# Optimization experiments

Hardware: AMD Instinct MI355X
Metric: run time of the kernel (lower is better)

Reference implementation:

```python
import jax, jax.numpy as jnp
import numpy as np

B, S, D = 2, 2048, 2048
H, KVH, HD = 16, 4, 128
NREP = H // KVH  # GQA repeat factor


def _rope(x, cos, sin):
    # x: [B,S,h,HD]; pairs (x[2k], x[2k+1]) form complex numbers
    xr = x[..., 0::2]
    xi = x[..., 1::2]
    cos = cos[None, :, None, :]  # [1,S,1,HD/2]
    sin = sin[None, :, None, :]
    out_r = xr * cos - xi * sin
    out_i = xr * sin + xi * cos
    return jnp.stack([out_r, out_i], axis=-1).reshape(x.shape)


def setup_inputs() -> dict:
    key = jax.random.key(0)
    ks = jax.random.split(key, 5)
    x = jax.random.normal(ks[0], (B, S, D), dtype=jnp.float32)
    # standard rotary frequencies
    inv_freq = 1.0 / (10000.0 ** (np.arange(0, HD, 2, dtype=np.float64) / HD))
    ang = np.outer(np.arange(S, dtype=np.float64), inv_freq)
    freqs_cos = jnp.asarray(np.cos(ang), dtype=jnp.float32)  # [S, HD/2]
    freqs_sin = jnp.asarray(np.sin(ang), dtype=jnp.float32)
    wq = jax.random.normal(ks[1], (D, H * HD), dtype=jnp.float32) * 0.02
    wk = jax.random.normal(ks[2], (D, KVH * HD), dtype=jnp.float32) * 0.02
    wv = jax.random.normal(ks[3], (D, KVH * HD), dtype=jnp.float32) * 0.02
    wo = jax.random.normal(ks[4], (H * HD, D), dtype=jnp.float32) * 0.02
    cache_k = jnp.zeros((B, S, KVH, HD), dtype=jnp.float32)
    cache_v = jnp.zeros((B, S, KVH, HD), dtype=jnp.float32)
    return {"x": x, "freqs_cos": freqs_cos, "freqs_sin": freqs_sin,
            "wq": wq, "wk": wk, "wv": wv, "wo": wo,
            "cache_k": cache_k, "cache_v": cache_v, "start_pos": 0}


def reference(x, freqs_cos, freqs_sin, wq, wk, wv, wo, cache_k, cache_v, start_pos):
    b, s, _ = x.shape
    xq = (x @ wq).reshape(b, s, H, HD)
    xk = (x @ wk).reshape(b, s, KVH, HD)
    xv = (x @ wv).reshape(b, s, KVH, HD)
    xq = _rope(xq, freqs_cos, freqs_sin)
    xk = _rope(xk, freqs_cos, freqs_sin)
    # KV cache update + slice (start_pos is a static Python int)
    ck = cache_k.at[:, start_pos:start_pos + s].set(xk)
    cv = cache_v.at[:, start_pos:start_pos + s].set(xv)
    keys = ck[:, :start_pos + s]    # [B,T,KVH,HD]
    vals = cv[:, :start_pos + s]
    # GQA without materializing repeat_kv: group query heads per kv head
    q = xq.reshape(b, s, KVH, NREP, HD)
    scores = jnp.einsum('bsknd,btkd->bknst', q, keys) / np.float32(np.sqrt(HD))
    probs = jax.nn.softmax(scores.astype(jnp.float32), axis=-1).astype(x.dtype)
    out = jnp.einsum('bknst,btkd->bsknd', probs, vals).reshape(b, s, H * HD)
    return out @ wo
```

## Files before the change

kernel.cpp:

```cpp
#include <hip/hip_runtime.h>
#include <stdint.h>
#include <stddef.h>

#define S_LEN  2048
#define NH     16
#define NKVH   4
#define HD_    128
#define DMODEL 2048
#define NQKV   3072
#define MROWS  4096

typedef __attribute__((ext_vector_type(8)))  __bf16 bf16x8;
typedef __attribute__((ext_vector_type(4)))  __bf16 bf16x4;
typedef __attribute__((ext_vector_type(4)))  float  f32x4;
typedef __attribute__((ext_vector_type(16))) float  f32x16;

#define MFMA16(a, b, c) __builtin_amdgcn_mfma_f32_16x16x32_bf16((a), (b), (c), 0, 0, 0)
#define MFMA32(a, b, c) __builtin_amdgcn_mfma_f32_32x32x16_bf16((a), (b), (c), 0, 0, 0)

__device__ __forceinline__ void gload16(const void* g, void* l) {
  __builtin_amdgcn_global_load_lds((const __attribute__((address_space(1))) void*)g,
                                   (__attribute__((address_space(3))) void*)l,
                                   16, 0, 0);
}

__device__ __forceinline__ float bf2f(uint16_t u) {
  uint32_t x = ((uint32_t)u) << 16;
  return __builtin_bit_cast(float, x);
}
__device__ __forceinline__ uint16_t f2bf(float f) {
  uint32_t u = __builtin_bit_cast(uint32_t, f);
  uint32_t r = (u + 0x7FFFu + ((u >> 16) & 1u)) >> 16;
  return (uint16_t)r;
}

__device__ __forceinline__ uint32_t cvtpk(float lo, float hi) {
  uint32_t d;
  asm("v_cvt_pk_bf16_f32 %0, %1, %2" : "=v"(d) : "v"(lo), "v"(hi));
  return d;
}
__device__ __forceinline__ void pswap(uint32_t& a, uint32_t& b) {
  asm("s_nop 1\n\tv_permlane32_swap_b32 %0, %1" : "+v"(a), "+v"(b));
}

__global__ void cvt_x_kernel(const float* __restrict__ x, __bf16* __restrict__ xb) {
  size_t i = (size_t)blockIdx.x * 256 + threadIdx.x;
  const float4* xv = (const float4*)x;
  float4 v = xv[i];
  bf16x4 o;
  o[0] = (__bf16)v.x; o[1] = (__bf16)v.y; o[2] = (__bf16)v.z; o[3] = (__bf16)v.w;
  *(bf16x4*)(xb + i * 4) = o;
}

__global__ void tw_kernel(const float* __restrict__ W, int ldw,
                          __bf16* __restrict__ WT, int ldt) {
  __shared__ float tile[64][65];
  const int k0 = blockIdx.x * 64, n0 = blockIdx.y * 64;
  const int tid = threadIdx.x;
#pragma unroll
  for (int r = 0; r < 16; ++r) {
    int idx = r * 256 + tid;
    int kr = idx >> 6, nc = idx & 63;
    tile[kr][nc] = W[(size_t)(k0 + kr) * ldw + n0 + nc];
  }
  __syncthreads();
#pragma unroll
  for (int r = 0; r < 16; ++r) {
    int idx = r * 256 + tid;
    int nr = idx >> 6, kc = idx & 63;
    WT[(size_t)(n0 + nr) * ldt + k0 + kc] = (__bf16)tile[kc][nr];
  }
}

template <int OUT_F32>
__global__ __launch_bounds__(256, 2) void gemm_kernel(
    const __bf16* __restrict__ A, int lda,
    const __bf16* __restrict__ Bt, int ldb,
    void* __restrict__ Cout, int ldc, int Kdim) {
  __shared__ __attribute__((aligned(16))) __bf16 As[128 * 64];
  __shared__ __attribute__((aligned(16))) __bf16 Bs[128 * 64];
  const int tid = threadIdx.x;
  const int w = tid >> 6, l = tid & 63, lg = l >> 4, lr = l & 15;
  const int wm = w >> 1, wn = w & 1;
  const int m0 = blockIdx.y * 128, n0 = blockIdx.x * 128;

  f32x4 acc[4][4] = {};

  for (int k0 = 0; k0 < Kdim; k0 += 64) {
#pragma unroll
    for (int t = 0; t < 4; ++t) {
      int o = (t * 256 + tid) * 16;
      int row = o >> 7;
      int slot = (o >> 4) & 7;
      int sw = slot ^ (row & 7);
      char* lbase = (char*)nullptr;
      lbase = (char*)As + t * 4096 + (w << 10);
      gload16(A + (size_t)(m0 + row) * lda + k0 + sw * 8, lbase);
      lbase = (char*)Bs + t * 4096 + (w << 10);
      gload16(Bt + (size_t)(n0 + row) * ldb + k0 + sw * 8, lbase);
    }
    __syncthreads();
#pragma unroll
    for (int c = 0; c < 2; ++c) {
      bf16x8 af[4];
#pragma unroll
      for (int mi = 0; mi < 4; ++mi) {
        int row = wm * 64 + mi * 16 + lr;
        int slot = (c * 4 + lg) ^ (row & 7);
        af[mi] = *(const bf16x8*)((const char*)As + row * 128 + slot * 16);
      }
#pragma unroll
      for (int ni = 0; ni < 4; ++ni) {
        int rn = wn * 64 + ni * 16 + lr;
        int slot = (c * 4 + lg) ^ (rn & 7);
        bf16x8 bfr = *(const bf16x8*)((const char*)Bs + rn * 128 + slot * 16);
#pragma unroll
        for (int mi = 0; mi < 4; ++mi)
          acc[mi][ni] = MFMA16(af[mi], bfr, acc[mi][ni]);
      }
    }
    __syncthreads();
  }

#pragma unroll
  for (int mi = 0; mi < 4; ++mi)
#pragma unroll
    for (int ni = 0; ni < 4; ++ni)
#pragma unroll
      for (int i = 0; i < 4; ++i) {
        int r = m0 + wm * 64 + mi * 16 + lg * 4 + i;
        int cc = n0 + wn * 64 + ni * 16 + lr;
        if (OUT_F32)
          ((float*)Cout)[(size_t)r * ldc + cc] = acc[mi][ni][i];
        else
          ((__bf16*)Cout)[(size_t)r * ldc + cc] = (__bf16)acc[mi][ni][i];
      }
}

__global__ void rope_kernel(__bf16* __restrict__ qkv,
                            const float* __restrict__ fc,
                            const float* __restrict__ fs) {
  const int row = blockIdx.x;
  const int s = row & (S_LEN - 1);
  const int tid = threadIdx.x;
  const float qscale = 0.08838834764831845f;
#pragma unroll
  for (int rep = 0; rep < 5; ++rep) {
    int pid = rep * 256 + tid;
    int col, j;
    float scale;
    if (pid < 1024) { int hh = pid >> 6; j = pid & 63; col = hh * HD_ + 2 * j; scale = qscale; }
    else { int p2 = pid - 1024; int kv = p2 >> 6; j = p2 & 63; col = DMODEL + kv * HD_ + 2 * j; scale = 1.0f; }
    uint32_t u = *(const uint32_t*)(qkv + (size_t)row * NQKV + col);
    float xr = bf2f((uint16_t)(u & 0xFFFFu));
    float xi = bf2f((uint16_t)(u >> 16));
    float c = fc[s * 64 + j], sn = fs[s * 64 + j];
    float orr = (xr * c - xi * sn) * scale;
    float oi  = (xr * sn + xi * c) * scale;
    uint32_t res = (uint32_t)f2bf(orr) | ((uint32_t)f2bf(oi) << 16);
    *(uint32_t*)(qkv + (size_t)row * NQKV + col) = res;
  }
}

__global__ void vt_kernel(const __bf16* __restrict__ qkv, __bf16* __restrict__ VT) {
  __shared__ uint16_t tile[64][66];
  const int bkv = blockIdx.z;
  const int b = bkv >> 2, kv = bkv & 3;
  const int s0 = blockIdx.x * 64, d0 = blockIdx.y * 64;
  const int tid = threadIdx.x;
#pragma unroll
  for (int r = 0; r < 16; ++r) {
    int idx = r * 256 + tid;
    int sr = idx >> 6, dc = idx & 63;
    tile[sr][dc] = *(const uint16_t*)(qkv + (size_t)(b * S_LEN + s0 + sr) * NQKV +
                                      (DMODEL + NKVH * HD_) + kv * HD_ + d0 + dc);
  }
  __syncthreads();
#pragma unroll
  for (int r = 0; r < 16; ++r) {
    int idx = r * 256 + tid;
    int dr = idx >> 6, sc = idx & 63;
    *(uint16_t*)(VT + (size_t)(bkv * HD_ + d0 + dr) * S_LEN + s0 + sc) = tile[sc][dr];
  }
}

__global__ __launch_bounds__(256, 2) void attn_kernel(
    const __bf16* __restrict__ qkv, const __bf16* __restrict__ VT,
    __bf16* __restrict__ out) {
  __shared__ __attribute__((aligned(16))) __bf16 Ks[64 * 128];
  __shared__ __attribute__((aligned(16))) __bf16 Vs[128 * 64];
  const int tid = threadIdx.x;
  const int w = tid >> 6, l = tid & 63;
  const int qc = l & 31, hi = l >> 5;
  const int bh = blockIdx.y;
  const int b = bh >> 4, h = bh & 15, kvh = h >> 2;
  const int q0 = blockIdx.x * 128 + w * 32;

  bf16x8 aq[8];
#pragma unroll
  for (int c = 0; c < 8; ++c)
    aq[c] = *(const bf16x8*)(qkv + (size_t)(b * S_LEN + q0 + qc) * NQKV +
                             h * HD_ + c * 16 + hi * 8);

  f32x16 o_acc[4] = {};
  float m = -1e30f, lsum = 0.0f;

  const __bf16* Kbase = qkv + (size_t)b * S_LEN * NQKV + DMODEL + kvh * HD_;
  const __bf16* Vbase = VT + (size_t)(b * NKVH + kvh) * (HD_ * S_LEN);

  typedef union { uint32_t u[4]; bf16x8 v; } pfrag_t;

  for (int kt = 0; kt < S_LEN / 64; ++kt) {
#pragma unroll
    for (int t = 0; t < 4; ++t) {
      int o = (t * 256 + tid) * 16;
      {
        int row = o >> 8; int slot = (o >> 4) & 15; int sw = slot ^ (row & 7);
        gload16(Kbase + (size_t)(kt * 64 + row) * NQKV + sw * 8,
                (char*)Ks + t * 4096 + (w << 10));
      }
      {
        int row = o >> 7; int slot = (o >> 4) & 7; int sw = slot ^ (row & 7);
        gload16(Vbase + (size_t)row * S_LEN + kt * 64 + sw * 8,
                (char*)Vs + t * 4096 + (w << 10));
      }
    }
    __syncthreads();

    f32x16 st[2] = {};
    __builtin_amdgcn_s_setprio(1);
#pragma unroll
    for (int t = 0; t < 2; ++t) {
#pragma unroll
      for (int c = 0; c < 8; ++c) {
        int row = t * 32 + qc;
        int slot = (c * 2 + hi) ^ (row & 7);
        bf16x8 kf = *(const bf16x8*)((const char*)Ks + row * 256 + slot * 16);
        st[t] = MFMA32(kf, aq[c], st[t]);
      }
    }
    __builtin_amdgcn_s_setprio(0);

    float pm = st[0][0];
#pragma unroll
    for (int t = 0; t < 2; ++t)
#pragma unroll
      for (int r = 0; r < 16; ++r) pm = fmaxf(pm, st[t][r]);
    pm = fmaxf(pm, __shfl_xor(pm, 32));

    if (__any(pm - m > 8.0f)) {
      float mn = fmaxf(m, pm);
      float sf = __expf(m - mn);
      lsum *= sf;
#pragma unroll
      for (int dt = 0; dt < 4; ++dt)
#pragma unroll
        for (int r = 0; r < 16; ++r) o_acc[dt][r] *= sf;
      m = mn;
    }

    float rsum = 0.0f;
#pragma unroll
    for (int t = 0; t < 2; ++t)
#pragma unroll
      for (int r = 0; r < 16; ++r) {
        st[t][r] = __expf(st[t][r] - m);
        rsum += st[t][r];
      }
    rsum += __shfl_xor(rsum, 32);
    lsum += rsum;

    pfrag_t pf[4];
#pragma unroll
    for (int t = 0; t < 2; ++t)
#pragma unroll
      for (int half = 0; half < 2; ++half) {
        int bs = half * 8;
        uint32_t x0 = cvtpk(st[t][bs + 0], st[t][bs + 1]);
        uint32_t y0 = cvtpk(st[t][bs + 4], st[t][bs + 5]);
        uint32_t x1 = cvtpk(st[t][bs + 2], st[t][bs + 3]);
        uint32_t y1 = cvtpk(st[t][bs + 6], st[t][bs + 7]);
        pswap(x0, y0);
        pswap(x1, y1);
        pf[t * 2 + half].u[0] = x0;
        pf[t * 2 + half].u[1] = x1;
        pf[t * 2 + half].u[2] = y0;
        pf[t * 2 + half].u[3] = y1;
      }

    __builtin_amdgcn_s_setprio(1);
#pragma unroll
    for (int dt = 0; dt < 4; ++dt) {
#pragma unroll
      for (int ks = 0; ks < 4; ++ks) {
        int row = dt * 32 + qc;
        int slot = (ks * 2 + hi) ^ (row & 7);
        bf16x8 vf = *(const bf16x8*)((const char*)Vs + row * 128 + slot * 16);
        o_acc[dt] = MFMA32(vf, pf[ks].v, o_acc[dt]);
      }
    }
    __builtin_amdgcn_s_setprio(0);
    __syncthreads();
  }

  float rinv = 1.0f / lsum;
  const size_t orow = (size_t)(b * S_LEN + q0 + qc) * DMODEL + h * HD_;
#pragma unroll
  for (int dt = 0; dt < 4; ++dt)
#pragma unroll
    for (int rg = 0; rg < 4; ++rg) {
      bf16x4 ov;
#pragma unroll
      for (int i = 0; i < 4; ++i)
        ov[i] = (__bf16)(o_acc[dt][rg * 4 + i] * rinv);
      int d = dt * 32 + rg * 8 + hi * 4;
      *(bf16x4*)(out + orow + d) = ov;
    }
}

extern "C" void kernel_launch(void* const* d_in, const int* in_sizes, int n_in,
                              void* d_out, int out_size, void* d_ws, size_t ws_size,
                              hipStream_t stream) {
  const float* x  = (const float*)d_in[0];
  const float* fc = (const float*)d_in[1];
  const float* fs = (const float*)d_in[2];
  const float* wq = (const float*)d_in[3];
  const float* wk = (const float*)d_in[4];
  const float* wv = (const float*)d_in[5];
  const float* wo = (const float*)d_in[6];

  char* ws = (char*)d_ws;
  __bf16* xb    = (__bf16*)(ws);
  __bf16* wqkvT = (__bf16*)(ws + (16u << 20));
  __bf16* woT   = (__bf16*)(ws + (28u << 20));
  __bf16* qkv   = (__bf16*)(ws + (36u << 20));
  __bf16* VT    = (__bf16*)(ws + (60u << 20));

  cvt_x_kernel<<<8192, 256, 0, stream>>>(x, xb);
  {
    dim3 g(32, 32); tw_kernel<<<g, 256, 0, stream>>>(wq, 2048, wqkvT, 2048);
  }
  {
    dim3 g(32, 8);
    tw_kernel<<<g, 256, 0, stream>>>(wk, 512, wqkvT + (size_t)2048 * 2048, 2048);
    tw_kernel<<<g, 256, 0, stream>>>(wv, 512, wqkvT + (size_t)2560 * 2048, 2048);
  }
  {
    dim3 g(32, 32); tw_kernel<<<g, 256, 0, stream>>>(wo, 2048, woT, 2048);
  }
  {
    dim3 g(NQKV / 128, MROWS / 128);
    gemm_kernel<0><<<g, 256, 0, stream>>>(xb, 2048, wqkvT, 2048, qkv, NQKV, 2048);
  }
  rope_kernel<<<MROWS, 256, 0, stream>>>(qkv, fc, fs);
  {
    dim3 g(32, 2, 8); vt_kernel<<<g, 256, 0, stream>>>(qkv, VT);
  }
  {
    dim3 g(S_LEN / 128, 32); attn_kernel<<<g, 256, 0, stream>>>(qkv, VT, xb);
  }
  {
    dim3 g(DMODEL / 128, MROWS / 128);
    gemm_kernel<1><<<g, 256, 0, stream>>>(xb, 2048, woT, 2048, d_out, 2048, 2048);
  }
}
```

Before: 204.9 us.

## Fuse prep kernels, fold RoPE into QKV GEMM, double-buffer attention, use exp2

Merges the x conversion and four weight-transpose launches into one prep kernel, and moves RoPE plus the query scale into the QKV GEMM epilogue so the separate rope pass over qkv is dropped. The query scale now includes log2(e), so the softmax uses exp2f, and the rescale threshold is adjusted to match. The attention kernel double-buffers its K and V shared-memory tiles, prefetching the next tile while computing the current one. This doubles attention LDS use, which may lower occupancy, and the RoPE epilogue does scattered loads of the cos/sin tables.

```diff
diff --git a/kernel.cpp b/kernel.cpp
--- a/kernel.cpp
+++ b/kernel.cpp
@@ -24,16 +24,6 @@
                                    16, 0, 0);
 }
 
-__device__ __forceinline__ float bf2f(uint16_t u) {
-  uint32_t x = ((uint32_t)u) << 16;
-  return __builtin_bit_cast(float, x);
-}
-__device__ __forceinline__ uint16_t f2bf(float f) {
-  uint32_t u = __builtin_bit_cast(uint32_t, f);
-  uint32_t r = (u + 0x7FFFu + ((u >> 16) & 1u)) >> 16;
-  return (uint16_t)r;
-}
-
 __device__ __forceinline__ uint32_t cvtpk(float lo, float hi) {
   uint32_t d;
   asm("v_cvt_pk_bf16_f32 %0, %1, %2" : "=v"(d) : "v"(lo), "v"(hi));
@@ -43,20 +33,29 @@
   asm("s_nop 1\n\tv_permlane32_swap_b32 %0, %1" : "+v"(a), "+v"(b));
 }
 
-__global__ void cvt_x_kernel(const float* __restrict__ x, __bf16* __restrict__ xb) {
-  size_t i = (size_t)blockIdx.x * 256 + threadIdx.x;
-  const float4* xv = (const float4*)x;
-  float4 v = xv[i];
-  bf16x4 o;
-  o[0] = (__bf16)v.x; o[1] = (__bf16)v.y; o[2] = (__bf16)v.z; o[3] = (__bf16)v.w;
-  *(bf16x4*)(xb + i * 4) = o;
-}
-
-__global__ void tw_kernel(const float* __restrict__ W, int ldw,
-                          __bf16* __restrict__ WT, int ldt) {
+__global__ void prep_kernel(const float* __restrict__ x, __bf16* __restrict__ xb,
+                            const float* __restrict__ wq, const float* __restrict__ wk,
+                            const float* __restrict__ wv, const float* __restrict__ wo,
+                            __bf16* __restrict__ wqkvT, __bf16* __restrict__ woT) {
   __shared__ float tile[64][65];
-  const int k0 = blockIdx.x * 64, n0 = blockIdx.y * 64;
+  const int bid = blockIdx.x;
   const int tid = threadIdx.x;
+  if (bid < 8192) {
+    size_t i = (size_t)bid * 256 + tid;
+    const float4* xv = (const float4*)x;
+    float4 v = xv[i];
+    bf16x4 o;
+    o[0] = (__bf16)v.x; o[1] = (__bf16)v.y; o[2] = (__bf16)v.z; o[3] = (__bf16)v.w;
+    *(bf16x4*)(xb + i * 4) = o;
+    return;
+  }
+  int b2 = bid - 8192;
+  const float* W; __bf16* WT; int ldw, kx, ny;
+  if (b2 < 1024)      { W = wq; WT = wqkvT;                        ldw = 2048; kx = b2 & 31; ny = b2 >> 5; }
+  else if (b2 < 1280) { int t = b2 - 1024; W = wk; WT = wqkvT + (size_t)2048 * 2048; ldw = 512; kx = t & 31; ny = t >> 5; }
+  else if (b2 < 1536) { int t = b2 - 1280; W = wv; WT = wqkvT + (size_t)2560 * 2048; ldw = 512; kx = t & 31; ny = t >> 5; }
+  else                { int t = b2 - 1536; W = wo; WT = woT;       ldw = 2048; kx = t & 31; ny = t >> 5; }
+  const int k0 = kx * 64, n0 = ny * 64;
 #pragma unroll
   for (int r = 0; r < 16; ++r) {
     int idx = r * 256 + tid;
@@ -68,15 +67,16 @@
   for (int r = 0; r < 16; ++r) {
     int idx = r * 256 + tid;
     int nr = idx >> 6, kc = idx & 63;
-    WT[(size_t)(n0 + nr) * ldt + k0 + kc] = (__bf16)tile[kc][nr];
-  }
-}
-
-template <int OUT_F32>
+    WT[(size_t)(n0 + nr) * 2048 + k0 + kc] = (__bf16)tile[kc][nr];
+  }
+}
+
+template <int OUT_F32, int DO_ROPE>
 __global__ __launch_bounds__(256, 2) void gemm_kernel(
     const __bf16* __restrict__ A, int lda,
     const __bf16* __restrict__ Bt, int ldb,
-    void* __restrict__ Cout, int ldc, int Kdim) {
+    void* __restrict__ Cout, int ldc, int Kdim,
+    const float* __restrict__ fc, const float* __restrict__ fs) {
   __shared__ __attribute__((aligned(16))) __bf16 As[128 * 64];
   __shared__ __attribute__((aligned(16))) __bf16 Bs[128 * 64];
   const int tid = threadIdx.x;
@@ -93,11 +93,10 @@
       int row = o >> 7;
       int slot = (o >> 4) & 7;
       int sw = slot ^ (row & 7);
-      char* lbase = (char*)nullptr;
-      lbase = (char*)As + t * 4096 + (w << 10);
-      gload16(A + (size_t)(m0 + row) * lda + k0 + sw * 8, lbase);
-      lbase = (char*)Bs + t * 4096 + (w << 10);
-      gload16(Bt + (size_t)(n0 + row) * ldb + k0 + sw * 8, lbase);
+      gload16(A + (size_t)(m0 + row) * lda + k0 + sw * 8,
+              (char*)As + t * 4096 + (w << 10));
+      gload16(Bt + (size_t)(n0 + row) * ldb + k0 + sw * 8,
+              (char*)Bs + t * 4096 + (w << 10));
     }
     __syncthreads();
 #pragma unroll
@@ -120,6 +119,29 @@
       }
     }
     __syncthreads();
+  }
+
+  if (DO_ROPE && n0 < 2560) {
+    const float qs = 0.12755102871936672f;
+#pragma unroll
+    for (int mi = 0; mi < 4; ++mi)
+#pragma unroll
+      for (int ni = 0; ni < 4; ++ni)
+#pragma unroll
+        for (int i = 0; i < 4; ++i) {
+          float v = acc[mi][ni][i];
+          float p = __shfl_xor(v, 1);
+          int cc = n0 + wn * 64 + ni * 16 + lr;
+          int r  = m0 + wm * 64 + mi * 16 + lg * 4 + i;
+          int s  = r & (S_LEN - 1);
+          int j  = (cc & 127) >> 1;
+          float c = fc[s * 64 + j], sn = fs[s * 64 + j];
+          float o = (lr & 1) ? (p * sn + v * c)
+                             : (v * c - p * sn);
+          if (cc < DMODEL) o *= qs;
+          ((__bf16*)Cout)[(size_t)r * ldc + cc] = (__bf16)o;
+        }
+    return;
   }
 
 #pragma unroll
@@ -137,31 +159,6 @@
       }
 }
 
-__global__ void rope_kernel(__bf16* __restrict__ qkv,
-                            const float* __restrict__ fc,
-                            const float* __restrict__ fs) {
-  const int row = blockIdx.x;
-  const int s = row & (S_LEN - 1);
-  const int tid = threadIdx.x;
-  const float qscale = 0.08838834764831845f;
-#pragma unroll
-  for (int rep = 0; rep < 5; ++rep) {
-    int pid = rep * 256 + tid;
-    int col, j;
-    float scale;
-    if (pid < 1024) { int hh = pid >> 6; j = pid & 63; col = hh * HD_ + 2 * j; scale = qscale; }
-    else { int p2 = pid - 1024; int kv = p2 >> 6; j = p2 & 63; col = DMODEL + kv * HD_ + 2 * j; scale = 1.0f; }
-    uint32_t u = *(const uint32_t*)(qkv + (size_t)row * NQKV + col);
-    float xr = bf2f((uint16_t)(u & 0xFFFFu));
-    float xi = bf2f((uint16_t)(u >> 16));
-    float c = fc[s * 64 + j], sn = fs[s * 64 + j];
-    float orr = (xr * c - xi * sn) * scale;
-    float oi  = (xr * sn + xi * c) * scale;
-    uint32_t res = (uint32_t)f2bf(orr) | ((uint32_t)f2bf(oi) << 16);
-    *(uint32_t*)(qkv + (size_t)row * NQKV + col) = res;
-  }
-}
-
 __global__ void vt_kernel(const __bf16* __restrict__ qkv, __bf16* __restrict__ VT) {
   __shared__ uint16_t tile[64][66];
   const int bkv = blockIdx.z;
@@ -187,8 +184,8 @@
 __global__ __launch_bounds__(256, 2) void attn_kernel(
     const __bf16* __restrict__ qkv, const __bf16* __restrict__ VT,
     __bf16* __restrict__ out) {
-  __shared__ __attribute__((aligned(16))) __bf16 Ks[64 * 128];
-  __shared__ __attribute__((aligned(16))) __bf16 Vs[128 * 64];
+  __shared__ __attribute__((aligned(16))) __bf16 Ks[2][64 * 128];
+  __shared__ __attribute__((aligned(16))) __bf16 Vs[2][128 * 64];
   const int tid = threadIdx.x;
   const int w = tid >> 6, l = tid & 63;
   const int qc = l & 31, hi = l >> 5;
@@ -196,36 +193,43 @@
   const int b = bh >> 4, h = bh & 15, kvh = h >> 2;
   const int q0 = blockIdx.x * 128 + w * 32;
 
-  bf16x8 aq[8];
-#pragma unroll
-  for (int c = 0; c < 8; ++c)
-    aq[c] = *(const bf16x8*)(qkv + (size_t)(b * S_LEN + q0 + qc) * NQKV +
-                             h * HD_ + c * 16 + hi * 8);
-
-  f32x16 o_acc[4] = {};
-  float m = -1e30f, lsum = 0.0f;
-
   const __bf16* Kbase = qkv + (size_t)b * S_LEN * NQKV + DMODEL + kvh * HD_;
   const __bf16* Vbase = VT + (size_t)(b * NKVH + kvh) * (HD_ * S_LEN);
 
-  typedef union { uint32_t u[4]; bf16x8 v; } pfrag_t;
-
-  for (int kt = 0; kt < S_LEN / 64; ++kt) {
+  auto stage = [&](int kt, int bufi) {
 #pragma unroll
     for (int t = 0; t < 4; ++t) {
       int o = (t * 256 + tid) * 16;
       {
         int row = o >> 8; int slot = (o >> 4) & 15; int sw = slot ^ (row & 7);
         gload16(Kbase + (size_t)(kt * 64 + row) * NQKV + sw * 8,
-                (char*)Ks + t * 4096 + (w << 10));
+                (char*)Ks[bufi] + t * 4096 + (w << 10));
       }
       {
         int row = o >> 7; int slot = (o >> 4) & 7; int sw = slot ^ (row & 7);
         gload16(Vbase + (size_t)row * S_LEN + kt * 64 + sw * 8,
-                (char*)Vs + t * 4096 + (w << 10));
-      }
-    }
-    __syncthreads();
+                (char*)Vs[bufi] + t * 4096 + (w << 10));
+      }
+    }
+  };
+
+  bf16x8 aq[8];
+#pragma unroll
+  for (int c = 0; c < 8; ++c)
+    aq[c] = *(const bf16x8*)(qkv + (size_t)(b * S_LEN + q0 + qc) * NQKV +
+                             h * HD_ + c * 16 + hi * 8);
+
+  f32x16 o_acc[4] = {};
+  float m = -1e30f, lsum = 0.0f;
+
+  typedef union { uint32_t u[4]; bf16x8 v; } pfrag_t;
+
+  stage(0, 0);
+  __syncthreads();
+  int buf = 0;
+
+  for (int kt = 0; kt < S_LEN / 64; ++kt) {
+    if (kt + 1 < S_LEN / 64) stage(kt + 1, buf ^ 1);
 
     f32x16 st[2] = {};
     __builtin_amdgcn_s_setprio(1);
@@ -235,7 +239,7 @@
       for (int c = 0; c < 8; ++c) {
         int row = t * 32 + qc;
         int slot = (c * 2 + hi) ^ (row & 7);
-        bf16x8 kf = *(const bf16x8*)((const char*)Ks + row * 256 + slot * 16);
+        bf16x8 kf = *(const bf16x8*)((const char*)Ks[buf] + row * 256 + slot * 16);
         st[t] = MFMA32(kf, aq[c], st[t]);
       }
     }
@@ -248,9 +252,9 @@
       for (int r = 0; r < 16; ++r) pm = fmaxf(pm, st[t][r]);
     pm = fmaxf(pm, __shfl_xor(pm, 32));
 
-    if (__any(pm - m > 8.0f)) {
+    if (__any(pm - m > 11.54f)) {
       float mn = fmaxf(m, pm);
-      float sf = __expf(m - mn);
+      float sf = exp2f(m - mn);
       lsum *= sf;
 #pragma unroll
       for (int dt = 0; dt < 4; ++dt)
@@ -264,7 +268,7 @@
     for (int t = 0; t < 2; ++t)
 #pragma unroll
       for (int r = 0; r < 16; ++r) {
-        st[t][r] = __expf(st[t][r] - m);
+        st[t][r] = exp2f(st[t][r] - m);
         rsum += st[t][r];
       }
     rsum += __shfl_xor(rsum, 32);
@@ -295,12 +299,13 @@
       for (int ks = 0; ks < 4; ++ks) {
         int row = dt * 32 + qc;
         int slot = (ks * 2 + hi) ^ (row & 7);
-        bf16x8 vf = *(const bf16x8*)((const char*)Vs + row * 128 + slot * 16);
+        bf16x8 vf = *(const bf16x8*)((const char*)Vs[buf] + row * 128 + slot * 16);
         o_acc[dt] = MFMA32(vf, pf[ks].v, o_acc[dt]);
       }
     }
     __builtin_amdgcn_s_setprio(0);
     __syncthreads();
+    buf ^= 1;
   }
 
   float rinv = 1.0f / lsum;
@@ -336,23 +341,11 @@
   __bf16* qkv   = (__bf16*)(ws + (36u << 20));
   __bf16* VT    = (__bf16*)(ws + (60u << 20));
 
-  cvt_x_kernel<<<8192, 256, 0, stream>>>(x, xb);
-  {
-    dim3 g(32, 32); tw_kernel<<<g, 256, 0, stream>>>(wq, 2048, wqkvT, 2048);
-  }
-  {
-    dim3 g(32, 8);
-    tw_kernel<<<g, 256, 0, stream>>>(wk, 512, wqkvT + (size_t)2048 * 2048, 2048);
-    tw_kernel<<<g, 256, 0, stream>>>(wv, 512, wqkvT + (size_t)2560 * 2048, 2048);
-  }
-  {
-    dim3 g(32, 32); tw_kernel<<<g, 256, 0, stream>>>(wo, 2048, woT, 2048);
-  }
+  prep_kernel<<<10752, 256, 0, stream>>>(x, xb, wq, wk, wv, wo, wqkvT, woT);
   {
     dim3 g(NQKV / 128, MROWS / 128);
-    gemm_kernel<0><<<g, 256, 0, stream>>>(xb, 2048, wqkvT, 2048, qkv, NQKV, 2048);
-  }
-  rope_kernel<<<MROWS, 256, 0, stream>>>(qkv, fc, fs);
+    gemm_kernel<0, 1><<<g, 256, 0, stream>>>(xb, 2048, wqkvT, 2048, qkv, NQKV, 2048, fc, fs);
+  }
   {
     dim3 g(32, 2, 8); vt_kernel<<<g, 256, 0, stream>>>(qkv, VT);
   }
@@ -361,6 +354,6 @@
   }
   {
     dim3 g(DMODEL / 128, MROWS / 128);
-    gemm_kernel<1><<<g, 256, 0, stream>>>(xb, 2048, woT, 2048, d_out, 2048, 2048);
-  }
-}
+    gemm_kernel<1, 0><<<g, 256, 0, stream>>>(xb, 2048, woT, 2048, d_out, 2048, 2048, fc, fs);
+  }
+}
```

Result: no change. 208.2 us (+1.6%).
